# Kernel optimization log

Measured on AMD Instinct MI355X. Metric: run time of the kernel, lower is better.

## Reference

```python
import jax, jax.numpy as jnp
import numpy as np

NQ = 10
EDGES = [[0, 1], [1, 2], [2, 3], [3, 4], [4, 5], [5, 6], [6, 7], [7, 8], [8, 9], [9, 0]]
RANGE = 2  # StronglyEntanglingLayers ranges=[2]
CRX_ANGLE = np.pi / 3.0  # trainBool=False -> constant angle

_c, _s = np.cos(CRX_ANGLE / 2), np.sin(CRX_ANGLE / 2)
CRX = np.array([[1, 0, 0, 0], [0, 1, 0, 0], [0, 0, _c, -1j * _s], [0, 0, -1j * _s, _c]], dtype=np.complex64)
CNOT = np.array([[1, 0, 0, 0], [0, 1, 0, 0], [0, 0, 0, 1], [0, 0, 1, 0]], dtype=np.complex64)


def _apply_1q(state, U, w):
    # state: (B, 2, ..., 2); U: (2,2) or batched (B,2,2)
    st = jnp.moveaxis(state, 1 + w, -1)
    if U.ndim == 3:
        st = jnp.einsum('b...i,bji->b...j', st, U)
    else:
        st = jnp.einsum('...i,ji->...j', st, U)
    return jnp.moveaxis(st, -1, 1 + w)


def _apply_2q(state, U, w1, w2):
    st = jnp.moveaxis(state, (1 + w1, 1 + w2), (-2, -1))
    shp = st.shape
    st = st.reshape(shp[:-2] + (4,))
    st = jnp.einsum('...i,ji->...j', st, U)
    return jnp.moveaxis(st.reshape(shp), (-2, -1), (1 + w1, 1 + w2))


def _ry_batch(theta):
    # per-sample RY gates, theta: (B,) -> (B,2,2)
    c, s = jnp.cos(theta / 2), jnp.sin(theta / 2)
    U = jnp.stack([jnp.stack([c, -s], -1), jnp.stack([s, c], -1)], -2)
    return U.astype(jnp.complex64)


def _rot(phi, theta, omega):
    # qml.Rot = RZ(omega) RY(theta) RZ(phi)
    c, s = jnp.cos(theta / 2), jnp.sin(theta / 2)
    u00 = jnp.exp(-0.5j * (phi + omega)) * c
    u01 = -jnp.exp(0.5j * (phi - omega)) * s
    u10 = jnp.exp(-0.5j * (phi - omega)) * s
    u11 = jnp.exp(0.5j * (phi + omega)) * c
    return jnp.stack([jnp.stack([u00, u01]), jnp.stack([u10, u11])]).astype(jnp.complex64)


def _circuit(inputs, weights):
    B = inputs.shape[0]
    state = jnp.zeros((B,) + (2,) * NQ, jnp.complex64)
    state = state.at[(slice(None),) + (0,) * NQ].set(1.0)
    # AngleEmbedding(rotation='Y')
    for w in range(NQ):
        state = _apply_1q(state, _ry_batch(inputs[:, w]), w)
    # CRX entanglers over the chain graph, angle pi/3
    for a, b in EDGES:
        state = _apply_2q(state, CRX, a, b)
    # StronglyEntanglingLayers, n_layers = weights.shape[0] = 1, range 2
    for l in range(weights.shape[0]):
        for i in range(NQ):
            state = _apply_1q(state, _rot(weights[l, i, 0], weights[l, i, 1], weights[l, i, 2]), i)
        for i in range(NQ):
            state = _apply_2q(state, CNOT, i, (i + RANGE) % NQ)
    # expval(PauliZ(i)) for each wire
    probs = state.real ** 2 + state.imag ** 2
    exps = []
    for i in range(NQ):
        axes = tuple(a for a in range(1, NQ + 1) if a != 1 + i)
        marg = probs.sum(axis=axes)  # (B, 2)
        exps.append(marg[:, 0] - marg[:, 1])
    return jnp.stack(exps, -1)  # (B, NQ)


def setup_inputs() -> dict:
    key = jax.random.key(0)
    k1, k2 = jax.random.split(key)
    inputs = jax.random.normal(k1, (8192, NQ), dtype=jnp.float32)
    weights = jax.random.uniform(k2, (1, NQ, 3), dtype=jnp.float32, minval=0.0, maxval=2 * np.pi)
    return {"inputs": inputs, "weights": weights}


def reference(inputs, weights):
    return _circuit(inputs, weights)
```

## Files before the change

kernel.cpp:

```cpp
#include <hip/hip_runtime.h>

#define NQ 10

struct cplx { float x, y; };
__device__ __forceinline__ cplx mk(float x, float y){ cplx c; c.x=x; c.y=y; return c; }
__device__ __forceinline__ cplx shflx(cplx a, int m){
    cplx r; r.x = __shfl_xor(a.x, m, 64); r.y = __shfl_xor(a.y, m, 64); return r;
}

template<int M, int R>
__device__ __forceinline__ void rot_reg(cplx (&a)[16], cplx u00, cplx u01, cplx u10, cplx u11){
    if constexpr (R < 16) {
        if constexpr ((R & M) == 0) {
            cplx a0 = a[R], a1 = a[R|M];
            a[R]   = mk(u00.x*a0.x - u00.y*a0.y + u01.x*a1.x - u01.y*a1.y,
                        u00.x*a0.y + u00.y*a0.x + u01.x*a1.y + u01.y*a1.x);
            a[R|M] = mk(u10.x*a0.x - u10.y*a0.y + u11.x*a1.x - u11.y*a1.y,
                        u10.x*a0.y + u10.y*a0.x + u11.x*a1.y + u11.y*a1.x);
        }
        rot_reg<M,R+1>(a, u00,u01,u10,u11);
    }
}

template<int LM, int R>
__device__ __forceinline__ void rot_lane(cplx (&a)[16], cplx ua, cplx ub){
    if constexpr (R < 16) {
        cplx p = shflx(a[R], LM);
        cplx m = a[R];
        a[R] = mk(ua.x*m.x - ua.y*m.y + ub.x*p.x - ub.y*p.y,
                  ua.x*m.y + ua.y*m.x + ub.x*p.y + ub.y*p.x);
        rot_lane<LM,R+1>(a, ua, ub);
    }
}


template<int MC, int MT, int R>
__device__ __forceinline__ void crx_rr(cplx (&a)[16], float cc, float ss){
    if constexpr (R < 16) {
        if constexpr ((R & MC) != 0 && (R & MT) == 0) {
            cplx a0 = a[R], a1 = a[R|MT];
            a[R]    = mk(cc*a0.x + ss*a1.y, cc*a0.y - ss*a1.x);
            a[R|MT] = mk(cc*a1.x + ss*a0.y, cc*a1.y - ss*a0.x);
        }
        crx_rr<MC,MT,R+1>(a, cc, ss);
    }
}

template<int MC, int LM, int R>
__device__ __forceinline__ void crx_rl(cplx (&a)[16], float cc, float ss){
    if constexpr (R < 16) {
        if constexpr ((R & MC) != 0) {
            cplx p = shflx(a[R], LM);
            cplx m = a[R];
            a[R] = mk(cc*m.x + ss*p.y, cc*m.y - ss*p.x);
        }
        crx_rl<MC,LM,R+1>(a, cc, ss);
    }
}

template<int MT, int R>
__device__ __forceinline__ void crx_lr(cplx (&a)[16], float al, float be){
    if constexpr (R < 16) {
        if constexpr ((R & MT) == 0) {
            cplx a0 = a[R], a1 = a[R|MT];
            a[R]    = mk(al*a0.x + be*a1.y, al*a0.y - be*a1.x);
            a[R|MT] = mk(al*a1.x + be*a0.y, al*a1.y - be*a0.x);
        }
        crx_lr<MT,R+1>(a, al, be);
    }
}

template<int TLM, int R>
__device__ __forceinline__ void crx_ll(cplx (&a)[16], float al, float be){
    if constexpr (R < 16) {
        cplx p = shflx(a[R], TLM);
        cplx m = a[R];
        a[R] = mk(al*m.x + be*p.y, al*m.y - be*p.x);
        crx_ll<TLM,R+1>(a, al, be);
    }
}

template<int R>
__device__ __forceinline__ void init_state(cplx (&a)[16], const float (&v)[16], float F){
    if constexpr (R < 16) {
        a[R] = mk(v[R] * F, 0.f);
        init_state<R+1>(a, v, F);
    }
}

template<int R>
__device__ __forceinline__ void accum4(const cplx (&a)[16], float &SA, float &SB, float &SC, float &SD){
    if constexpr (R < 16) {
        float p = a[R].x*a[R].x + a[R].y*a[R].y;
        SA += ((R>>2) & 1)            ? -p : p;
        SB += ((R>>3) & 1)            ? -p : p;
        SC += ((R ^ (R>>2)) & 1)      ? -p : p;
        SD += (((R>>1) ^ (R>>3)) & 1) ? -p : p;
        accum4<R+1>(a, SA, SB, SC, SD);
    }
}

__device__ __forceinline__ float wave_sum(float v){
    v += __shfl_xor(v,  1, 64);
    v += __shfl_xor(v,  2, 64);
    v += __shfl_xor(v,  4, 64);
    v += __shfl_xor(v,  8, 64);
    v += __shfl_xor(v, 16, 64);
    v += __shfl_xor(v, 32, 64);
    return v;
}

__device__ __forceinline__ float fsgn(float v, unsigned s){
    return __uint_as_float(__float_as_uint(v) ^ s);
}
__device__ __forceinline__ unsigned parsgn(int lane, int m){
    return (unsigned)((__builtin_popcount(lane & m) & 1)) << 31;
}

__global__ void prep_gates(const float* __restrict__ weights, float* __restrict__ gates){
    int i = threadIdx.x;
    if (i < NQ) {
        float phi = weights[i*3 + 0], th = weights[i*3 + 1], om = weights[i*3 + 2];
        float ct, st, ca, sa, cb, sb;
        __sincosf(0.5f * th, &st, &ct);
        __sincosf(0.5f * (phi + om), &sa, &ca);
        __sincosf(0.5f * (phi - om), &sb, &cb);
        float* g = gates + i*8;
        g[0] =  ct*ca; g[1] = -ct*sa;
        g[2] = -st*cb; g[3] = -st*sb;
        g[4] =  st*cb; g[5] = -st*sb;
        g[6] =  ct*ca; g[7] =  ct*sa;
    }
}

__global__ __launch_bounds__(256) void qsim_kernel(const float* __restrict__ inputs,
                                                   const float* __restrict__ gates,
                                                   float* __restrict__ out, int B){
    const int lane = threadIdx.x & 63;
    const int wave = __builtin_amdgcn_readfirstlane((int)((blockIdx.x * blockDim.x + threadIdx.x) >> 6));
    if (wave >= B) return;

    const float* ang = inputs + (size_t)wave * NQ;

    float c[NQ], s[NQ];
    #pragma unroll
    for (int w = 0; w < NQ; ++w) __sincosf(0.5f * ang[w], &s[w], &c[w]);

    float F = 1.f;
    F *= (lane &  1) ? s[4] : c[4];
    F *= (lane &  2) ? s[5] : c[5];
    F *= (lane &  4) ? s[6] : c[6];
    F *= (lane &  8) ? s[7] : c[7];
    F *= (lane & 16) ? s[8] : c[8];
    F *= (lane & 32) ? s[9] : c[9];

    float v2[2]  = { c[0], s[0] };
    float v4[4]  = { v2[0]*c[1], v2[1]*c[1], v2[0]*s[1], v2[1]*s[1] };
    float v8[8]  = { v4[0]*c[2], v4[1]*c[2], v4[2]*c[2], v4[3]*c[2],
                     v4[0]*s[2], v4[1]*s[2], v4[2]*s[2], v4[3]*s[2] };
    float v16[16];
    #pragma unroll
    for (int r = 0; r < 8; ++r) { v16[r] = v8[r]*c[3]; v16[r+8] = v8[r]*s[3]; }

    cplx amp[16];
    init_state<0>(amp, v16, F);

    const float cc = 0.86602540378443864676f;
    const float ss = 0.5f;
    crx_rr<1, 2, 0>(amp, cc, ss);
    crx_rr<2, 4, 0>(amp, cc, ss);
    crx_rr<4, 8, 0>(amp, cc, ss);
    crx_rl<8, 1, 0>(amp, cc, ss);
    { bool t = (lane &  1); crx_ll< 2,0>(amp, t?cc:1.f, t?ss:0.f); }
    { bool t = (lane &  2); crx_ll< 4,0>(amp, t?cc:1.f, t?ss:0.f); }
    { bool t = (lane &  4); crx_ll< 8,0>(amp, t?cc:1.f, t?ss:0.f); }
    { bool t = (lane &  8); crx_ll<16,0>(amp, t?cc:1.f, t?ss:0.f); }
    { bool t = (lane & 16); crx_ll<32,0>(amp, t?cc:1.f, t?ss:0.f); }
    { bool t = (lane & 32); crx_lr< 1,0>(amp, t?cc:1.f, t?ss:0.f); }

    #define GG(i) mk(gates[(i)*8+0],gates[(i)*8+1]), mk(gates[(i)*8+2],gates[(i)*8+3]), \
                  mk(gates[(i)*8+4],gates[(i)*8+5]), mk(gates[(i)*8+6],gates[(i)*8+7])
    rot_reg<1, 0>(amp, GG(0));
    rot_reg<2, 0>(amp, GG(1));
    rot_reg<4, 0>(amp, GG(2));
    rot_reg<8, 0>(amp, GG(3));
    #undef GG
    #pragma unroll
    for (int w = 4; w < NQ; ++w) {
        const float* g = gates + w*8;
        bool hi = (lane & (1 << (w-4))) != 0;
        cplx ua = mk(hi ? g[6] : g[0], hi ? g[7] : g[1]);
        cplx ub = mk(hi ? g[4] : g[2], hi ? g[5] : g[3]);
        switch (w) {
            case 4: rot_lane< 1,0>(amp, ua, ub); break;
            case 5: rot_lane< 2,0>(amp, ua, ub); break;
            case 6: rot_lane< 4,0>(amp, ua, ub); break;
            case 7: rot_lane< 8,0>(amp, ua, ub); break;
            case 8: rot_lane<16,0>(amp, ua, ub); break;
            case 9: rot_lane<32,0>(amp, ua, ub); break;
        }
    }

    float SA = 0.f, SB = 0.f, SC = 0.f, SD = 0.f;
    accum4<0>(amp, SA, SB, SC, SD);

    unsigned p1  = parsgn(lane,  1), p2  = parsgn(lane,  2);
    unsigned p5  = parsgn(lane,  5), p10 = parsgn(lane, 10);
    unsigned p21 = parsgn(lane, 21), p42 = parsgn(lane, 42);

    float r0 = wave_sum(fsgn(SA, p21));
    float r1 = wave_sum(fsgn(SB, p42));
    float r2 = wave_sum(SC);
    float r3 = wave_sum(SD);
    float r4 = wave_sum(fsgn(SC, p1));
    float r5 = wave_sum(fsgn(SD, p2));
    float r6 = wave_sum(fsgn(SC, p5));
    float r7 = wave_sum(fsgn(SD, p10));
    float r8 = wave_sum(fsgn(SC, p21));
    float r9 = wave_sum(fsgn(SD, p42));

    if (lane == 0) {
        float* o = out + (size_t)wave * NQ;
        o[0] = r0; o[1] = r1; o[2] = r2; o[3] = r3; o[4] = r4;
        o[5] = r5; o[6] = r6; o[7] = r7; o[8] = r8; o[9] = r9;
    }
}

extern "C" void kernel_launch(void* const* d_in, const int* in_sizes, int n_in,
                              void* d_out, int out_size, void* d_ws, size_t ws_size,
                              hipStream_t stream) {
    const float* inputs  = (const float*)d_in[0];
    const float* weights = (const float*)d_in[1];
    float* out   = (float*)d_out;
    float* gates = (float*)d_ws;
    const int B = in_sizes[0] / NQ;

    prep_gates<<<1, 64, 0, stream>>>(weights, gates);

    const int wavesPerBlock = 256 / 64;
    const int blocks = (B + wavesPerBlock - 1) / wavesPerBlock;
    qsim_kernel<<<blocks, 256, 0, stream>>>(inputs, gates, out, B);
}
```

Before: 99.10 us.

## Fuse gate preparation into simulation kernel and drop separate prep launch

Removes the prep_gates kernel and has each wave compute the Rot gate coefficients from the weights inline. It also folds the per-lane factor F into the first amplitude product and sets launch bounds to ask for 8 blocks per CU. This saves one kernel launch and the dependency between the two launches, in exchange for redundant sincos work in every wave and possible register-pressure changes from the occupancy hint.

```diff
diff --git a/kernel.cpp b/kernel.cpp
--- a/kernel.cpp
+++ b/kernel.cpp
@@ -80,11 +80,22 @@
     }
 }
 
-template<int R>
-__device__ __forceinline__ void init_state(cplx (&a)[16], const float (&v)[16], float F){
-    if constexpr (R < 16) {
-        a[R] = mk(v[R] * F, 0.f);
-        init_state<R+1>(a, v, F);
+template<int I>
+__device__ __forceinline__ void do_rot(cplx (&amp)[16], int lane, const float* __restrict__ w){
+    float phi = w[I*3 + 0], th = w[I*3 + 1], om = w[I*3 + 2];
+    float ct, st, ca, sa, cb, sb;
+    __sincosf(0.5f * th, &st, &ct);
+    __sincosf(0.5f * (phi + om), &sa, &ca);
+    __sincosf(0.5f * (phi - om), &sb, &cb);
+    float A = ct*ca, Bv = ct*sa, C = st*cb, D = st*sb;
+    if constexpr (I < 4) {
+        rot_reg<(1<<I),0>(amp, mk(A,-Bv), mk(-C,-D), mk(C,-D), mk(A,Bv));
+    } else {
+        constexpr int LM = 1 << (I - 4);
+        const bool hi = (lane & LM) != 0;
+        cplx ua = mk(A, hi ? Bv : -Bv);
+        cplx ub = mk(hi ? C : -C, -D);
+        rot_lane<LM,0>(amp, ua, ub);
     }
 }
 
@@ -117,53 +128,43 @@
     return (unsigned)((__builtin_popcount(lane & m) & 1)) << 31;
 }
 
-__global__ void prep_gates(const float* __restrict__ weights, float* __restrict__ gates){
-    int i = threadIdx.x;
-    if (i < NQ) {
-        float phi = weights[i*3 + 0], th = weights[i*3 + 1], om = weights[i*3 + 2];
-        float ct, st, ca, sa, cb, sb;
-        __sincosf(0.5f * th, &st, &ct);
-        __sincosf(0.5f * (phi + om), &sa, &ca);
-        __sincosf(0.5f * (phi - om), &sb, &cb);
-        float* g = gates + i*8;
-        g[0] =  ct*ca; g[1] = -ct*sa;
-        g[2] = -st*cb; g[3] = -st*sb;
-        g[4] =  st*cb; g[5] = -st*sb;
-        g[6] =  ct*ca; g[7] =  ct*sa;
-    }
-}
-
-__global__ __launch_bounds__(256) void qsim_kernel(const float* __restrict__ inputs,
-                                                   const float* __restrict__ gates,
-                                                   float* __restrict__ out, int B){
+__global__ __launch_bounds__(256, 8) void qsim_kernel(const float* __restrict__ inputs,
+                                                      const float* __restrict__ weights,
+                                                      float* __restrict__ out, int B){
     const int lane = threadIdx.x & 63;
     const int wave = __builtin_amdgcn_readfirstlane((int)((blockIdx.x * blockDim.x + threadIdx.x) >> 6));
     if (wave >= B) return;
 
     const float* ang = inputs + (size_t)wave * NQ;
 
-    float c[NQ], s[NQ];
+    float F = 1.f;
+    {
+        float s, c;
+        __sincosf(0.5f * ang[4], &s, &c); F *= (lane &  1) ? s : c;
+        __sincosf(0.5f * ang[5], &s, &c); F *= (lane &  2) ? s : c;
+        __sincosf(0.5f * ang[6], &s, &c); F *= (lane &  4) ? s : c;
+        __sincosf(0.5f * ang[7], &s, &c); F *= (lane &  8) ? s : c;
+        __sincosf(0.5f * ang[8], &s, &c); F *= (lane & 16) ? s : c;
+        __sincosf(0.5f * ang[9], &s, &c); F *= (lane & 32) ? s : c;
+    }
+
+    float c0,s0,c1,s1,c2,s2,c3,s3;
+    __sincosf(0.5f * ang[0], &s0, &c0);
+    __sincosf(0.5f * ang[1], &s1, &c1);
+    __sincosf(0.5f * ang[2], &s2, &c2);
+    __sincosf(0.5f * ang[3], &s3, &c3);
+
+    float v2a = F * c0, v2b = F * s0;
+    float v4[4] = { v2a*c1, v2b*c1, v2a*s1, v2b*s1 };
+    float v8[8] = { v4[0]*c2, v4[1]*c2, v4[2]*c2, v4[3]*c2,
+                    v4[0]*s2, v4[1]*s2, v4[2]*s2, v4[3]*s2 };
+
+    cplx amp[16];
     #pragma unroll
-    for (int w = 0; w < NQ; ++w) __sincosf(0.5f * ang[w], &s[w], &c[w]);
-
-    float F = 1.f;
-    F *= (lane &  1) ? s[4] : c[4];
-    F *= (lane &  2) ? s[5] : c[5];
-    F *= (lane &  4) ? s[6] : c[6];
-    F *= (lane &  8) ? s[7] : c[7];
-    F *= (lane & 16) ? s[8] : c[8];
-    F *= (lane & 32) ? s[9] : c[9];
-
-    float v2[2]  = { c[0], s[0] };
-    float v4[4]  = { v2[0]*c[1], v2[1]*c[1], v2[0]*s[1], v2[1]*s[1] };
-    float v8[8]  = { v4[0]*c[2], v4[1]*c[2], v4[2]*c[2], v4[3]*c[2],
-                     v4[0]*s[2], v4[1]*s[2], v4[2]*s[2], v4[3]*s[2] };
-    float v16[16];
-    #pragma unroll
-    for (int r = 0; r < 8; ++r) { v16[r] = v8[r]*c[3]; v16[r+8] = v8[r]*s[3]; }
-
-    cplx amp[16];
-    init_state<0>(amp, v16, F);
+    for (int r = 0; r < 8; ++r) {
+        amp[r]   = mk(v8[r] * c3, 0.f);
+        amp[r+8] = mk(v8[r] * s3, 0.f);
+    }
 
     const float cc = 0.86602540378443864676f;
     const float ss = 0.5f;
@@ -178,28 +179,16 @@
     { bool t = (lane & 16); crx_ll<32,0>(amp, t?cc:1.f, t?ss:0.f); }
     { bool t = (lane & 32); crx_lr< 1,0>(amp, t?cc:1.f, t?ss:0.f); }
 
-    #define GG(i) mk(gates[(i)*8+0],gates[(i)*8+1]), mk(gates[(i)*8+2],gates[(i)*8+3]), \
-                  mk(gates[(i)*8+4],gates[(i)*8+5]), mk(gates[(i)*8+6],gates[(i)*8+7])
-    rot_reg<1, 0>(amp, GG(0));
-    rot_reg<2, 0>(amp, GG(1));
-    rot_reg<4, 0>(amp, GG(2));
-    rot_reg<8, 0>(amp, GG(3));
-    #undef GG
-    #pragma unroll
-    for (int w = 4; w < NQ; ++w) {
-        const float* g = gates + w*8;
-        bool hi = (lane & (1 << (w-4))) != 0;
-        cplx ua = mk(hi ? g[6] : g[0], hi ? g[7] : g[1]);
-        cplx ub = mk(hi ? g[4] : g[2], hi ? g[5] : g[3]);
-        switch (w) {
-            case 4: rot_lane< 1,0>(amp, ua, ub); break;
-            case 5: rot_lane< 2,0>(amp, ua, ub); break;
-            case 6: rot_lane< 4,0>(amp, ua, ub); break;
-            case 7: rot_lane< 8,0>(amp, ua, ub); break;
-            case 8: rot_lane<16,0>(amp, ua, ub); break;
-            case 9: rot_lane<32,0>(amp, ua, ub); break;
-        }
-    }
+    do_rot<0>(amp, lane, weights);
+    do_rot<1>(amp, lane, weights);
+    do_rot<2>(amp, lane, weights);
+    do_rot<3>(amp, lane, weights);
+    do_rot<4>(amp, lane, weights);
+    do_rot<5>(amp, lane, weights);
+    do_rot<6>(amp, lane, weights);
+    do_rot<7>(amp, lane, weights);
+    do_rot<8>(amp, lane, weights);
+    do_rot<9>(amp, lane, weights);
 
     float SA = 0.f, SB = 0.f, SC = 0.f, SD = 0.f;
     accum4<0>(amp, SA, SB, SC, SD);
@@ -231,13 +220,9 @@
                               hipStream_t stream) {
     const float* inputs  = (const float*)d_in[0];
     const float* weights = (const float*)d_in[1];
-    float* out   = (float*)d_out;
-    float* gates = (float*)d_ws;
+    float* out = (float*)d_out;
     const int B = in_sizes[0] / NQ;
-
-    prep_gates<<<1, 64, 0, stream>>>(weights, gates);
-
     const int wavesPerBlock = 256 / 64;
     const int blocks = (B + wavesPerBlock - 1) / wavesPerBlock;
-    qsim_kernel<<<blocks, 256, 0, stream>>>(inputs, gates, out, B);
-}
+    qsim_kernel<<<blocks, 256, 0, stream>>>(inputs, weights, out, B);
+}
```

Measured after the change: 395.4 us. +299.0%, slower.
